# Performance work log

Hardware: AMD Instinct MI355X
Metric: run time of the kernel (lower is better)

Reference implementation:

```python
import jax, jax.numpy as jnp
import numpy as np

B, T, D, H, DH, W = 2, 2048, 512, 8, 64, 64  # batch, seq, d_model, heads, d_head, window
BASE = 10000.0


def rope(x):
    # x: [b, t, d]; rotate-half RoPE applied over the full feature dim (as in source: pos_enc on d_model)
    d = x.shape[-1]
    half = d // 2
    inv_freq = BASE ** (-jnp.arange(half, dtype=jnp.float32) / half)          # [half]
    ang = jnp.arange(x.shape[1], dtype=jnp.float32)[:, None] * inv_freq       # [t, half]
    cos, sin = jnp.cos(ang), jnp.sin(ang)
    x1, x2 = x[..., :half], x[..., half:]
    return jnp.concatenate([x1 * cos - x2 * sin, x1 * sin + x2 * cos], axis=-1)


def setup_inputs() -> dict:
    key = jax.random.key(0)
    k0, k1, k2, k3 = jax.random.split(key, 4)
    x = jax.random.normal(k0, (B, T, D), jnp.float32)
    Wq = jax.random.normal(k1, (D, D), jnp.float32) / jnp.sqrt(D)
    Wkv = jax.random.normal(k2, (D, 2 * D), jnp.float32) / jnp.sqrt(D)
    # NOTE: source zero-inits lin; we use random weights so the output/grads are non-trivial
    Wlin = jax.random.normal(k3, (D, D), jnp.float32) / jnp.sqrt(D)
    blin = jnp.zeros((D,), jnp.float32)
    return {"x": x, "Wq": Wq, "Wkv": Wkv, "Wlin": Wlin, "blin": blin}


def reference(x, Wq, Wkv, Wlin, blin):
    b, t, _ = x.shape
    scale = DH ** -0.5
    q = rope(x @ Wq).reshape(b, t, H, DH).transpose(0, 2, 1, 3)               # [b,h,t,d]
    kv = x @ Wkv
    k, v = kv[..., :D], kv[..., D:]
    k = rope(k).reshape(b, t, H, DH).transpose(0, 2, 1, 3)                    # [b,h,t,d]
    v = v.reshape(b, t, H, DH).transpose(0, 2, 1, 3)                          # [b,h,t,d]
    pad = [(0, 0), (0, 0), (W - 1, 0), (0, 0)]
    kp, vp = jnp.pad(k, pad), jnp.pad(v, pad)                                 # [b,h,t+W-1,d]
    idx = jnp.arange(t)[:, None] + jnp.arange(W)[None, :]                     # [t,W] sliding-window gather
    kw, vw = kp[:, :, idx], vp[:, :, idx]                                     # [b,h,t,W,d]
    attn = jax.nn.softmax(jnp.einsum('bhtd,bhtwd->bhtw', q, kw) * scale, axis=-1)
    out = jnp.einsum('bhtw,bhtwd->bhtd', attn, vw)                            # [b,h,t,d]
    out = out.transpose(0, 2, 1, 3).reshape(b, t, D)
    return out @ Wlin + blin
```

## Files before the change

kernel.cpp:

```cpp
#include <hip/hip_runtime.h>
#include <cstddef>

#define T_N 2048
#define D_N 512
#define H_N 8
#define M_N 4096
#define KP  512

typedef __attribute__((ext_vector_type(4))) float f32x4;
typedef _Float16 f16x8 __attribute__((ext_vector_type(8)));
typedef _Float16 f16x4 __attribute__((ext_vector_type(4)));

#define GLOAD_LDS(g, l) __builtin_amdgcn_global_load_lds( \
    (const __attribute__((address_space(1))) unsigned int*)(g), \
    (__attribute__((address_space(3))) unsigned int*)(l), 16, 0, 0)

__global__ __launch_bounds__(256) void trig_kernel(float* __restrict__ tab) {
  int idx = blockIdx.x * blockDim.x + threadIdx.x;
  int t = idx >> 8, f = idx & 255;
  float invf = exp2f(-0.05190512648261503f * (float)f);
  float ang = (float)t * invf;
  float s, c;
  sincosf(ang, &s, &c);
  tab[t * 512 + f] = c;
  tab[t * 512 + 256 + f] = s;
}

__global__ __launch_bounds__(256) void pack_all(
    const float* __restrict__ x, const float* __restrict__ Wq,
    const float* __restrict__ Wkv, const float* __restrict__ Wlin,
    _Float16* __restrict__ Axp, _Float16* __restrict__ Wcatp,
    _Float16* __restrict__ Wlinp) {
  __shared__ float tile[64][65];
  int bid = blockIdx.x;
  const int tid = threadIdx.x;
  if (bid < 1024) {
    int idx = bid * 256 + tid;
    int m = idx >> 6, k8 = (idx & 63) << 3;
    const float* src = x + (size_t)m * 512 + k8;
    const float4 a = *(const float4*)src;
    const float4 b = *(const float4*)(src + 4);
    f16x8 o;
    o[0] = (_Float16)a.x; o[1] = (_Float16)a.y; o[2] = (_Float16)a.z; o[3] = (_Float16)a.w;
    o[4] = (_Float16)b.x; o[5] = (_Float16)b.y; o[6] = (_Float16)b.z; o[7] = (_Float16)b.w;
    *(f16x8*)(Axp + (size_t)m * 512 + k8) = o;
    return;
  }
  bid -= 1024;
  const float* W; int N; _Float16* out; int bx, by;
  if (bid < 64)       { W = Wq;   N = 512;  out = Wcatp;                        bx = bid & 7;  by = bid >> 3; }
  else if (bid < 192) { bid -= 64;  W = Wkv; N = 1024; out = Wcatp + (size_t)512 * KP; bx = bid & 15; by = bid >> 4; }
  else                { bid -= 192; W = Wlin; N = 512; out = Wlinp;             bx = bid & 7;  by = bid >> 3; }
  const int n0 = bx * 64, k0 = by * 64;
#pragma unroll
  for (int it = 0; it < 16; ++it) {
    int idx = tid + it * 256;
    int r = idx >> 6, c = idx & 63;
    tile[r][c] = W[(size_t)(k0 + r) * N + n0 + c];
  }
  __syncthreads();
#pragma unroll
  for (int it = 0; it < 16; ++it) {
    int idx = tid + it * 256;
    int n = idx >> 6, kk = idx & 63;
    out[(size_t)(n0 + n) * KP + k0 + kk] = (_Float16)tile[kk][n];
  }
}

__global__ __launch_bounds__(256) void gemm_mfma(
    const _Float16* __restrict__ Ap, const _Float16* __restrict__ Bp,
    float* __restrict__ C, int ldc, const float* __restrict__ bias) {
  __shared__ __align__(16) _Float16 sA[128 * 64];
  __shared__ __align__(16) _Float16 sB[128 * 64];
  const int tid = threadIdx.x;
  const int wid = tid >> 6, lane = tid & 63;
  const int m0 = blockIdx.y * 128, n0 = blockIdx.x * 128;
  const int wm = (wid >> 1) * 64, wn = (wid & 1) * 64;
  f32x4 acc[4][4] = {};

  const int srow = wid * 32 + (lane >> 3);
  const int scol = (lane & 7) * 8;
  const _Float16* ga = Ap + (size_t)(m0 + srow) * KP + scol;
  const _Float16* gb = Bp + (size_t)(n0 + srow) * KP + scol;
  _Float16* la = &sA[wid * 32 * 64];
  _Float16* lb = &sB[wid * 32 * 64];

  for (int k0 = 0; k0 < KP; k0 += 64) {
#pragma unroll
    for (int i = 0; i < 4; ++i) {
      GLOAD_LDS(ga + (size_t)(i * 8) * KP + k0, la + i * 8 * 64);
      GLOAD_LDS(gb + (size_t)(i * 8) * KP + k0, lb + i * 8 * 64);
    }
    __syncthreads();
#pragma unroll
    for (int ks = 0; ks < 2; ++ks) {
      f16x8 af[4], bfr[4];
#pragma unroll
      for (int i = 0; i < 4; ++i) {
        af[i]  = *(const f16x8*)&sA[(wm + i * 16 + (lane & 15)) * 64 + ks * 32 + (lane >> 4) * 8];
        bfr[i] = *(const f16x8*)&sB[(wn + i * 16 + (lane & 15)) * 64 + ks * 32 + (lane >> 4) * 8];
      }
#pragma unroll
      for (int i = 0; i < 4; ++i)
#pragma unroll
        for (int j = 0; j < 4; ++j)
          acc[i][j] = __builtin_amdgcn_mfma_f32_16x16x32_f16(af[i], bfr[j], acc[i][j], 0, 0, 0);
    }
    __syncthreads();
  }
  const int cn = n0 + wn + (lane & 15);
  const int rbase = m0 + wm + (lane >> 4) * 4;
#pragma unroll
  for (int j = 0; j < 4; ++j) {
    float badd = bias ? bias[cn + j * 16] : 0.f;
#pragma unroll
    for (int i = 0; i < 4; ++i)
#pragma unroll
      for (int r = 0; r < 4; ++r)
        C[(size_t)(rbase + i * 16 + r) * ldc + cn + j * 16] = acc[i][j][r] + badd;
  }
}

__global__ __launch_bounds__(256) void rope_pack(
    const float* __restrict__ qkv, const float* __restrict__ tab,
    _Float16* __restrict__ Qh, _Float16* __restrict__ Kh,
    _Float16* __restrict__ Vh) {
  int bid = blockIdx.x;
  const int tid = threadIdx.x;
  if (bid < 2048) {
    int idx = bid * 256 + tid;
    int which = idx >> 18;
    int r = idx & ((1 << 18) - 1);
    int m = r >> 6;
    int c4 = (r & 63) << 2;
    int t = m & (T_N - 1);
    int b = m >> 11;
    const float* base = qkv + (size_t)m * 1536 + (which ? 512 : 0);
    const float4 v1 = *(const float4*)(base + c4);
    const float4 v2 = *(const float4*)(base + c4 + 256);
    const float4 ct = *(const float4*)(tab + (size_t)t * 512 + c4);
    const float4 st = *(const float4*)(tab + (size_t)t * 512 + 256 + c4);
    f16x4 o1, o2;
    o1[0] = (_Float16)(v1.x * ct.x - v2.x * st.x);  o2[0] = (_Float16)(v1.x * st.x + v2.x * ct.x);
    o1[1] = (_Float16)(v1.y * ct.y - v2.y * st.y);  o2[1] = (_Float16)(v1.y * st.y + v2.y * ct.y);
    o1[2] = (_Float16)(v1.z * ct.z - v2.z * st.z);  o2[2] = (_Float16)(v1.z * st.z + v2.z * ct.z);
    o1[3] = (_Float16)(v1.w * ct.w - v2.w * st.w);  o2[3] = (_Float16)(v1.w * st.w + v2.w * ct.w);
    _Float16* dst = which ? Kh : Qh;
    int h1 = c4 >> 6, d1 = c4 & 63;
    *(f16x4*)(dst + ((size_t)(b * 8 + h1) * T_N + t) * 64 + d1) = o1;
    *(f16x4*)(dst + ((size_t)(b * 8 + h1 + 4) * T_N + t) * 64 + d1) = o2;
    return;
  }
  bid -= 2048;
  __shared__ _Float16 vt[64][72];
  const int b = bid >> 8, h = (bid >> 5) & 7, tt = bid & 31;
  const int t0 = tt * 64;
#pragma unroll
  for (int it = 0; it < 16; ++it) {
    int idx = tid + it * 256;
    int tl = idx >> 6, d = idx & 63;
    vt[d][tl] = (_Float16)qkv[(size_t)(b * T_N + t0 + tl) * 1536 + 1024 + h * 64 + d];
  }
  __syncthreads();
#pragma unroll
  for (int it = 0; it < 2; ++it) {
    int idx = tid + it * 256;
    int d = idx >> 3, tc = (idx & 7) * 8;
    *(f16x8*)(Vh + ((size_t)(b * 8 + h) * 64 + d) * T_N + t0 + tc) =
        *(const f16x8*)&vt[d][tc];
  }
}

#define RQ 72
#define RK 72
#define RV 104
#define RP 104
#define RO 72

__global__ __launch_bounds__(256, 4) void attn_fused(
    const _Float16* __restrict__ Qh, const _Float16* __restrict__ Kh,
    const _Float16* __restrict__ Vh, _Float16* __restrict__ Aout) {
  __shared__ __align__(16) _Float16 sm[19200];
  __shared__ float pm[2][32];
  __shared__ float ps[2][32];
  _Float16* Ks  = sm;
  _Float16* Qs  = sm + 6912;
  _Float16* VTs = sm + 9216;
  _Float16* Ps  = sm + 15872;
  _Float16* OH  = sm;

  const int wgid = blockIdx.x;
  const int orig = (wgid & 7) * 128 + (wgid >> 3);
  const int tile = orig & 63;
  const int h = (orig >> 6) & 7;
  const int b = orig >> 9;
  const int t0 = tile * 32;
  const int tid = threadIdx.x;
  const size_t bh = (size_t)(b * 8 + h);

  {
    int i = tid >> 3, d8 = (tid & 7) * 8;
    *(f16x8*)(Qs + i * RQ + d8) =
        *(const f16x8*)(Qh + (bh * T_N + t0 + i) * 64 + d8);
  }
#pragma unroll
  for (int itn = 0; itn < 3; ++itn) {
    int c = tid + itn * 256;
    int jr = c >> 3, d8 = (c & 7) * 8;
    int p = t0 - 64 + jr;
    f16x8 o = {};
    if (p >= 0) o = *(const f16x8*)(Kh + (bh * T_N + p) * 64 + d8);
    *(f16x8*)(Ks + jr * RK + d8) = o;
  }
#pragma unroll
  for (int itn = 0; itn < 3; ++itn) {
    int c = tid + itn * 256;
    int d = c & 63, ci = c >> 6 + 0;
    ci = (c >> 6);
    int jr8 = ci * 8;
    int p8 = t0 - 64 + jr8;
    f16x8 o = {};
    if (p8 >= 0) o = *(const f16x8*)(Vh + (bh * 64 + d) * T_N + p8);
    *(f16x8*)(VTs + d * RV + jr8) = o;
  }
  __syncthreads();

  const int lane = tid & 63;
  const int il = lane & 15, g = lane >> 4;
  const int w = tid >> 6;
  const int it = w & 1, jh = w >> 1;
  const int i_q = 16 * it + il;

  f32x4 sacc[3] = {};
  {
    f16x8 qf0 = *(const f16x8*)(Qs + i_q * RQ + 8 * g);
    f16x8 qf1 = *(const f16x8*)(Qs + i_q * RQ + 32 + 8 * g);
#pragma unroll
    for (int jt = 0; jt < 3; ++jt) {
      int jrow = 16 * (3 * jh + jt) + il;
      f16x8 a0 = *(const f16x8*)(Ks + jrow * RK + 8 * g);
      f16x8 a1 = *(const f16x8*)(Ks + jrow * RK + 32 + 8 * g);
      sacc[jt] = __builtin_amdgcn_mfma_f32_16x16x32_f16(a0, qf0, sacc[jt], 0, 0, 0);
      sacc[jt] = __builtin_amdgcn_mfma_f32_16x16x32_f16(a1, qf1, sacc[jt], 0, 0, 0);
    }
  }
  float mx = -3e38f;
#pragma unroll
  for (int jt = 0; jt < 3; ++jt)
#pragma unroll
    for (int r = 0; r < 4; ++r) {
      int j = 16 * (3 * jh + jt) + 4 * g + r;
      int wv = j - 1 - i_q;
      if (wv >= 0 && wv < 64) mx = fmaxf(mx, sacc[jt][r]);
    }
  mx = fmaxf(mx, __shfl_xor(mx, 16));
  mx = fmaxf(mx, __shfl_xor(mx, 32));
  if (g == 0) pm[jh][i_q] = mx;
  __syncthreads();
  {
    const float m = fmaxf(pm[0][i_q], pm[1][i_q]);
    float sum = 0.f;
#pragma unroll
    for (int jt = 0; jt < 3; ++jt)
#pragma unroll
      for (int r = 0; r < 4; ++r) {
        int j = 16 * (3 * jh + jt) + 4 * g + r;
        int wv = j - 1 - i_q;
        float ex = 0.f;
        if (wv >= 0 && wv < 64) {
          ex = exp2f((sacc[jt][r] - m) * 0.18033688011112042f);
          sum += ex;
        }
        Ps[i_q * RP + j] = (_Float16)ex;
      }
    sum += __shfl_xor(sum, 16);
    sum += __shfl_xor(sum, 32);
    if (g == 0) ps[jh][i_q] = sum;
  }
  __syncthreads();

  f32x4 oacc[2] = {};
#pragma unroll
  for (int ks = 0; ks < 3; ++ks) {
    f16x8 pf = *(const f16x8*)(Ps + i_q * RP + 32 * ks + 8 * g);
#pragma unroll
    for (int q2 = 0; q2 < 2; ++q2) {
      int dt = jh + 2 * q2;
      f16x8 vf = *(const f16x8*)(VTs + (16 * dt + il) * RV + 32 * ks + 8 * g);
      oacc[q2] = __builtin_amdgcn_mfma_f32_16x16x32_f16(pf, vf, oacc[q2], 0, 0, 0);
    }
  }
#pragma unroll
  for (int r = 0; r < 4; ++r) {
    int i = 16 * it + 4 * g + r;
    float inv = 1.f / (ps[0][i] + ps[1][i]);
#pragma unroll
    for (int q2 = 0; q2 < 2; ++q2) {
      int d = 16 * (jh + 2 * q2) + il;
      OH[i * RO + d] = (_Float16)(oacc[q2][r] * inv);
    }
  }
  __syncthreads();
  {
    int i = tid >> 3, d8 = (tid & 7) * 8;
    *(f16x8*)(Aout + ((size_t)(b * T_N + t0 + i)) * 512 + h * 64 + d8) =
        *(const f16x8*)(OH + i * RO + d8);
  }
}

extern "C" void kernel_launch(void* const* d_in, const int* in_sizes, int n_in,
                              void* d_out, int out_size, void* d_ws, size_t ws_size,
                              hipStream_t stream) {
  const float* x    = (const float*)d_in[0];
  const float* Wq   = (const float*)d_in[1];
  const float* Wkv  = (const float*)d_in[2];
  const float* Wlin = (const float*)d_in[3];
  const float* blin = (const float*)d_in[4];
  float* out = (float*)d_out;

  char* ws = (char*)d_ws;
  float*     qkvbuf = (float*)(ws);
  float*     tab    = (float*)(ws + 25165824);
  _Float16*  Axp    = (_Float16*)(ws + 29360128);
  _Float16*  Wcatp  = (_Float16*)(ws + 33554432);
  _Float16*  Wlinp  = (_Float16*)(ws + 35127296);
  _Float16*  Qh     = (_Float16*)(ws + 35651584);
  _Float16*  Kh     = (_Float16*)(ws + 39845888);
  _Float16*  Vh     = (_Float16*)(ws + 44040192);
  _Float16*  Aaop   = (_Float16*)(ws + 48234496);

  trig_kernel<<<T_N, 256, 0, stream>>>(tab);
  pack_all<<<1280, 256, 0, stream>>>(x, Wq, Wkv, Wlin, Axp, Wcatp, Wlinp);
  gemm_mfma<<<dim3(12, 32), 256, 0, stream>>>(Axp, Wcatp, qkvbuf, 1536, nullptr);
  rope_pack<<<2560, 256, 0, stream>>>(qkvbuf, tab, Qh, Kh, Vh);
  attn_fused<<<1024, 256, 0, stream>>>(Qh, Kh, Vh, Aaop);
  gemm_mfma<<<dim3(4, 32), 256, 0, stream>>>(Aaop, Wlinp, out, 512, blin);
}
```

Baseline: 116.2 us.

## Fuse RoPE into QKV GEMM epilogue, merge trig into prep, shrink GEMM tiles

Permutes the Wq/Wk columns during weight packing so that each RoPE pair (f, f+256) sits in adjacent output columns. RoPE can then run in the QKV GEMM epilogue using a lane shuffle, writing fp16 Q/K head-major directly instead of going through an fp32 qkv buffer. The trig table is now fp16 and is generated inside the prep kernel, which removes one launch. V is written as fp16 and transposed by a separate small kernel. Both GEMMs use smaller tiles to put more blocks in flight. The risks are extra fp16 rounding in the sin/cos values and scattered 2-byte epilogue stores.

New measurement: 112.0 us. 1.04x faster.

```diff
diff --git a/kernel.cpp b/kernel.cpp
--- a/kernel.cpp
+++ b/kernel.cpp
@@ -2,37 +2,24 @@
 #include <cstddef>
 
 #define T_N 2048
-#define D_N 512
-#define H_N 8
 #define M_N 4096
-#define KP  512
+#define KW  512
 
 typedef __attribute__((ext_vector_type(4))) float f32x4;
 typedef _Float16 f16x8 __attribute__((ext_vector_type(8)));
-typedef _Float16 f16x4 __attribute__((ext_vector_type(4)));
+typedef _Float16 f16x2 __attribute__((ext_vector_type(2)));
 
 #define GLOAD_LDS(g, l) __builtin_amdgcn_global_load_lds( \
     (const __attribute__((address_space(1))) unsigned int*)(g), \
     (__attribute__((address_space(3))) unsigned int*)(l), 16, 0, 0)
 
-__global__ __launch_bounds__(256) void trig_kernel(float* __restrict__ tab) {
-  int idx = blockIdx.x * blockDim.x + threadIdx.x;
-  int t = idx >> 8, f = idx & 255;
-  float invf = exp2f(-0.05190512648261503f * (float)f);
-  float ang = (float)t * invf;
-  float s, c;
-  sincosf(ang, &s, &c);
-  tab[t * 512 + f] = c;
-  tab[t * 512 + 256 + f] = s;
-}
-
-__global__ __launch_bounds__(256) void pack_all(
+__global__ __launch_bounds__(256) void prep(
     const float* __restrict__ x, const float* __restrict__ Wq,
     const float* __restrict__ Wkv, const float* __restrict__ Wlin,
     _Float16* __restrict__ Axp, _Float16* __restrict__ Wcatp,
-    _Float16* __restrict__ Wlinp) {
+    _Float16* __restrict__ Wlinp, _Float16* __restrict__ tab16) {
   __shared__ float tile[64][65];
-  int bid = blockIdx.x;
+  const int bid = blockIdx.x;
   const int tid = threadIdx.x;
   if (bid < 1024) {
     int idx = bid * 256 + tid;
@@ -46,11 +33,22 @@
     *(f16x8*)(Axp + (size_t)m * 512 + k8) = o;
     return;
   }
-  bid -= 1024;
-  const float* W; int N; _Float16* out; int bx, by;
-  if (bid < 64)       { W = Wq;   N = 512;  out = Wcatp;                        bx = bid & 7;  by = bid >> 3; }
-  else if (bid < 192) { bid -= 64;  W = Wkv; N = 1024; out = Wcatp + (size_t)512 * KP; bx = bid & 15; by = bid >> 4; }
-  else                { bid -= 192; W = Wlin; N = 512; out = Wlinp;             bx = bid & 7;  by = bid >> 3; }
+  if (bid >= 1280) {
+    int gid = (bid - 1280) * 256 + tid;
+    int t = gid >> 8, f = gid & 255;
+    float invf = exp2f(-0.05190512648261503f * (float)f);
+    float s, c;
+    sincosf((float)t * invf, &s, &c);
+    f16x2 cs;
+    cs[0] = (_Float16)c; cs[1] = (_Float16)s;
+    *(f16x2*)(tab16 + 2 * ((size_t)t * 256 + f)) = cs;
+    return;
+  }
+  int wb = bid - 1024;
+  const float* W; int N; int mode; int bx, by;
+  if (wb < 64)       { W = Wq;   N = 512;  mode = 0; bx = wb & 7;  by = wb >> 3; }
+  else if (wb < 192) { wb -= 64;  W = Wkv; N = 1024; mode = 1; bx = wb & 15; by = wb >> 4; }
+  else               { wb -= 192; W = Wlin; N = 512; mode = 2; bx = wb & 7;  by = wb >> 3; }
   const int n0 = bx * 64, k0 = by * 64;
 #pragma unroll
   for (int it = 0; it < 16; ++it) {
@@ -63,103 +61,104 @@
   for (int it = 0; it < 16; ++it) {
     int idx = tid + it * 256;
     int n = idx >> 6, kk = idx & 63;
-    out[(size_t)(n0 + n) * KP + k0 + kk] = (_Float16)tile[kk][n];
-  }
-}
-
-__global__ __launch_bounds__(256) void gemm_mfma(
+    int cg = n0 + n;
+    int np; _Float16* out;
+    if (mode == 0)      { np = 2 * (cg & 255) + (cg >> 8); out = Wcatp; }
+    else if (mode == 1) { np = (cg < 512) ? 512 + 2 * (cg & 255) + (cg >> 8)
+                                          : 1024 + (cg - 512);
+                          out = Wcatp; }
+    else                { np = cg; out = Wlinp; }
+    out[(size_t)np * KW + k0 + kk] = (_Float16)tile[kk][n];
+  }
+}
+
+__global__ __launch_bounds__(256) void gemm_qkv_rope(
     const _Float16* __restrict__ Ap, const _Float16* __restrict__ Bp,
-    float* __restrict__ C, int ldc, const float* __restrict__ bias) {
-  __shared__ __align__(16) _Float16 sA[128 * 64];
+    const _Float16* __restrict__ tab16, _Float16* __restrict__ Qh,
+    _Float16* __restrict__ Kh, _Float16* __restrict__ Vn) {
+  __shared__ __align__(16) _Float16 sA[64 * 64];
   __shared__ __align__(16) _Float16 sB[128 * 64];
   const int tid = threadIdx.x;
   const int wid = tid >> 6, lane = tid & 63;
-  const int m0 = blockIdx.y * 128, n0 = blockIdx.x * 128;
-  const int wm = (wid >> 1) * 64, wn = (wid & 1) * 64;
-  f32x4 acc[4][4] = {};
-
-  const int srow = wid * 32 + (lane >> 3);
-  const int scol = (lane & 7) * 8;
-  const _Float16* ga = Ap + (size_t)(m0 + srow) * KP + scol;
-  const _Float16* gb = Bp + (size_t)(n0 + srow) * KP + scol;
-  _Float16* la = &sA[wid * 32 * 64];
-  _Float16* lb = &sB[wid * 32 * 64];
-
-  for (int k0 = 0; k0 < KP; k0 += 64) {
-#pragma unroll
-    for (int i = 0; i < 4; ++i) {
-      GLOAD_LDS(ga + (size_t)(i * 8) * KP + k0, la + i * 8 * 64);
-      GLOAD_LDS(gb + (size_t)(i * 8) * KP + k0, lb + i * 8 * 64);
-    }
+  const int il = lane & 15, g = lane >> 4;
+  const int m0 = blockIdx.y * 64, n0 = blockIdx.x * 128;
+  const int wm = (wid >> 1) * 32, wn = (wid & 1) * 64;
+  f32x4 acc[2][4] = {};
+
+  const _Float16* ga = Ap + (size_t)(m0 + wid * 16 + (lane >> 3)) * KW + (lane & 7) * 8;
+  const _Float16* gb = Bp + (size_t)(n0 + wid * 32 + (lane >> 3)) * KW + (lane & 7) * 8;
+  _Float16* la = sA + wid * 16 * 64;
+  _Float16* lb = sB + wid * 32 * 64;
+
+  for (int k0 = 0; k0 < KW; k0 += 64) {
+    GLOAD_LDS(ga + k0, la);
+    GLOAD_LDS(ga + 8 * KW + k0, la + 8 * 64);
+#pragma unroll
+    for (int p = 0; p < 4; ++p)
+      GLOAD_LDS(gb + (size_t)(p * 8) * KW + k0, lb + p * 8 * 64);
     __syncthreads();
 #pragma unroll
     for (int ks = 0; ks < 2; ++ks) {
-      f16x8 af[4], bfr[4];
-#pragma unroll
-      for (int i = 0; i < 4; ++i) {
-        af[i]  = *(const f16x8*)&sA[(wm + i * 16 + (lane & 15)) * 64 + ks * 32 + (lane >> 4) * 8];
-        bfr[i] = *(const f16x8*)&sB[(wn + i * 16 + (lane & 15)) * 64 + ks * 32 + (lane >> 4) * 8];
+      f16x8 af[2], bf[4];
+#pragma unroll
+      for (int i = 0; i < 2; ++i)
+        af[i] = *(const f16x8*)&sA[(wm + i * 16 + il) * 64 + ks * 32 + g * 8];
+#pragma unroll
+      for (int j = 0; j < 4; ++j)
+        bf[j] = *(const f16x8*)&sB[(wn + j * 16 + il) * 64 + ks * 32 + g * 8];
+#pragma unroll
+      for (int i = 0; i < 2; ++i)
+#pragma unroll
+        for (int j = 0; j < 4; ++j)
+          acc[i][j] = __builtin_amdgcn_mfma_f32_16x16x32_f16(af[i], bf[j], acc[i][j], 0, 0, 0);
+    }
+    __syncthreads();
+  }
+  const int b8 = (m0 >> 11) * 8;
+  const bool isv = (n0 >= 1024);
+  const bool isk = (n0 >= 512) && !isv;
+  const int n0p = n0 - (isk ? 512 : 0);
+#pragma unroll
+  for (int i = 0; i < 2; ++i) {
+#pragma unroll
+    for (int j = 0; j < 4; ++j) {
+      f32x4 v = acc[i][j];
+#pragma unroll
+      for (int r = 0; r < 4; ++r) {
+        float self = v[r];
+        float part = __shfl_xor(self, 1);
+        int tl = wm + i * 16 + g * 4 + r;
+        int tpos = (m0 + tl) & (T_N - 1);
+        if (isv) {
+          Vn[(size_t)(m0 + tl) * 512 + (n0 - 1024) + wn + il + 16 * j] = (_Float16)self;
+        } else {
+          int p = il & 1;
+          int f = (n0p + wn + 16 * j + (il & 14)) >> 1;
+          f16x2 cs = *(const f16x2*)(tab16 + 2 * ((size_t)tpos * 256 + f));
+          float c = (float)cs[0], s = (float)cs[1];
+          float o = p ? (self * c + part * s) : (self * c - part * s);
+          int h = (f >> 6) + (p << 2);
+          int d = f & 63;
+          _Float16* dst = isk ? Kh : Qh;
+          dst[((size_t)(b8 + h) * T_N + tpos) * 64 + d] = (_Float16)o;
+        }
       }
-#pragma unroll
-      for (int i = 0; i < 4; ++i)
-#pragma unroll
-        for (int j = 0; j < 4; ++j)
-          acc[i][j] = __builtin_amdgcn_mfma_f32_16x16x32_f16(af[i], bfr[j], acc[i][j], 0, 0, 0);
-    }
-    __syncthreads();
-  }
-  const int cn = n0 + wn + (lane & 15);
-  const int rbase = m0 + wm + (lane >> 4) * 4;
-#pragma unroll
-  for (int j = 0; j < 4; ++j) {
-    float badd = bias ? bias[cn + j * 16] : 0.f;
-#pragma unroll
-    for (int i = 0; i < 4; ++i)
-#pragma unroll
-      for (int r = 0; r < 4; ++r)
-        C[(size_t)(rbase + i * 16 + r) * ldc + cn + j * 16] = acc[i][j][r] + badd;
-  }
-}
-
-__global__ __launch_bounds__(256) void rope_pack(
-    const float* __restrict__ qkv, const float* __restrict__ tab,
-    _Float16* __restrict__ Qh, _Float16* __restrict__ Kh,
-    _Float16* __restrict__ Vh) {
-  int bid = blockIdx.x;
-  const int tid = threadIdx.x;
-  if (bid < 2048) {
-    int idx = bid * 256 + tid;
-    int which = idx >> 18;
-    int r = idx & ((1 << 18) - 1);
-    int m = r >> 6;
-    int c4 = (r & 63) << 2;
-    int t = m & (T_N - 1);
-    int b = m >> 11;
-    const float* base = qkv + (size_t)m * 1536 + (which ? 512 : 0);
-    const float4 v1 = *(const float4*)(base + c4);
-    const float4 v2 = *(const float4*)(base + c4 + 256);
-    const float4 ct = *(const float4*)(tab + (size_t)t * 512 + c4);
-    const float4 st = *(const float4*)(tab + (size_t)t * 512 + 256 + c4);
-    f16x4 o1, o2;
-    o1[0] = (_Float16)(v1.x * ct.x - v2.x * st.x);  o2[0] = (_Float16)(v1.x * st.x + v2.x * ct.x);
-    o1[1] = (_Float16)(v1.y * ct.y - v2.y * st.y);  o2[1] = (_Float16)(v1.y * st.y + v2.y * ct.y);
-    o1[2] = (_Float16)(v1.z * ct.z - v2.z * st.z);  o2[2] = (_Float16)(v1.z * st.z + v2.z * ct.z);
-    o1[3] = (_Float16)(v1.w * ct.w - v2.w * st.w);  o2[3] = (_Float16)(v1.w * st.w + v2.w * ct.w);
-    _Float16* dst = which ? Kh : Qh;
-    int h1 = c4 >> 6, d1 = c4 & 63;
-    *(f16x4*)(dst + ((size_t)(b * 8 + h1) * T_N + t) * 64 + d1) = o1;
-    *(f16x4*)(dst + ((size_t)(b * 8 + h1 + 4) * T_N + t) * 64 + d1) = o2;
-    return;
-  }
-  bid -= 2048;
+    }
+  }
+}
+
+__global__ __launch_bounds__(256) void vtrans(
+    const _Float16* __restrict__ Vn, _Float16* __restrict__ Vh) {
   __shared__ _Float16 vt[64][72];
+  const int bid = blockIdx.x;
+  const int tid = threadIdx.x;
   const int b = bid >> 8, h = (bid >> 5) & 7, tt = bid & 31;
   const int t0 = tt * 64;
 #pragma unroll
   for (int it = 0; it < 16; ++it) {
     int idx = tid + it * 256;
     int tl = idx >> 6, d = idx & 63;
-    vt[d][tl] = (_Float16)qkv[(size_t)(b * T_N + t0 + tl) * 1536 + 1024 + h * 64 + d];
+    vt[d][tl] = Vn[(size_t)(b * T_N + t0 + tl) * 512 + h * 64 + d];
   }
   __syncthreads();
 #pragma unroll
@@ -215,9 +214,7 @@
 #pragma unroll
   for (int itn = 0; itn < 3; ++itn) {
     int c = tid + itn * 256;
-    int d = c & 63, ci = c >> 6 + 0;
-    ci = (c >> 6);
-    int jr8 = ci * 8;
+    int d = c & 63, jr8 = (c >> 6) * 8;
     int p8 = t0 - 64 + jr8;
     f16x8 o = {};
     if (p8 >= 0) o = *(const f16x8*)(Vh + (bh * 64 + d) * T_N + p8);
@@ -308,6 +305,59 @@
   }
 }
 
+__global__ __launch_bounds__(256) void gemm_out(
+    const _Float16* __restrict__ Ap, const _Float16* __restrict__ Bp,
+    const float* __restrict__ bias, float* __restrict__ C) {
+  __shared__ __align__(16) _Float16 sA[64 * 64];
+  __shared__ __align__(16) _Float16 sB[64 * 64];
+  const int tid = threadIdx.x;
+  const int wid = tid >> 6, lane = tid & 63;
+  const int il = lane & 15, g = lane >> 4;
+  const int m0 = blockIdx.y * 64, n0 = blockIdx.x * 64;
+  const int wm = (wid >> 1) * 32, wn = (wid & 1) * 32;
+  f32x4 acc[2][2] = {};
+
+  const _Float16* ga = Ap + (size_t)(m0 + wid * 16 + (lane >> 3)) * KW + (lane & 7) * 8;
+  const _Float16* gb = Bp + (size_t)(n0 + wid * 16 + (lane >> 3)) * KW + (lane & 7) * 8;
+  _Float16* la = sA + wid * 16 * 64;
+  _Float16* lb = sB + wid * 16 * 64;
+
+  for (int k0 = 0; k0 < KW; k0 += 64) {
+    GLOAD_LDS(ga + k0, la);
+    GLOAD_LDS(ga + 8 * KW + k0, la + 8 * 64);
+    GLOAD_LDS(gb + k0, lb);
+    GLOAD_LDS(gb + 8 * KW + k0, lb + 8 * 64);
+    __syncthreads();
+#pragma unroll
+    for (int ks = 0; ks < 2; ++ks) {
+      f16x8 af[2], bf[2];
+#pragma unroll
+      for (int i = 0; i < 2; ++i)
+        af[i] = *(const f16x8*)&sA[(wm + i * 16 + il) * 64 + ks * 32 + g * 8];
+#pragma unroll
+      for (int j = 0; j < 2; ++j)
+        bf[j] = *(const f16x8*)&sB[(wn + j * 16 + il) * 64 + ks * 32 + g * 8];
+#pragma unroll
+      for (int i = 0; i < 2; ++i)
+#pragma unroll
+        for (int j = 0; j < 2; ++j)
+          acc[i][j] = __builtin_amdgcn_mfma_f32_16x16x32_f16(af[i], bf[j], acc[i][j], 0, 0, 0);
+    }
+    __syncthreads();
+  }
+  const int cn = n0 + wn + il;
+  const int rbase = m0 + wm + g * 4;
+#pragma unroll
+  for (int j = 0; j < 2; ++j) {
+    float badd = bias[cn + j * 16];
+#pragma unroll
+    for (int i = 0; i < 2; ++i)
+#pragma unroll
+      for (int r = 0; r < 4; ++r)
+        C[(size_t)(rbase + i * 16 + r) * 512 + cn + j * 16] = acc[i][j][r] + badd;
+  }
+}
+
 extern "C" void kernel_launch(void* const* d_in, const int* in_sizes, int n_in,
                               void* d_out, int out_size, void* d_ws, size_t ws_size,
                               hipStream_t stream) {
@@ -319,20 +369,19 @@
   float* out = (float*)d_out;
 
   char* ws = (char*)d_ws;
-  float*     qkvbuf = (float*)(ws);
-  float*     tab    = (float*)(ws + 25165824);
-  _Float16*  Axp    = (_Float16*)(ws + 29360128);
-  _Float16*  Wcatp  = (_Float16*)(ws + 33554432);
-  _Float16*  Wlinp  = (_Float16*)(ws + 35127296);
-  _Float16*  Qh     = (_Float16*)(ws + 35651584);
-  _Float16*  Kh     = (_Float16*)(ws + 39845888);
-  _Float16*  Vh     = (_Float16*)(ws + 44040192);
-  _Float16*  Aaop   = (_Float16*)(ws + 48234496);
-
-  trig_kernel<<<T_N, 256, 0, stream>>>(tab);
-  pack_all<<<1280, 256, 0, stream>>>(x, Wq, Wkv, Wlin, Axp, Wcatp, Wlinp);
-  gemm_mfma<<<dim3(12, 32), 256, 0, stream>>>(Axp, Wcatp, qkvbuf, 1536, nullptr);
-  rope_pack<<<2560, 256, 0, stream>>>(qkvbuf, tab, Qh, Kh, Vh);
+  _Float16* Axp   = (_Float16*)(ws);
+  _Float16* Wcatp = (_Float16*)(ws + 4194304);
+  _Float16* Wlinp = (_Float16*)(ws + 5767168);
+  _Float16* tab16 = (_Float16*)(ws + 6291456);
+  _Float16* Qh    = (_Float16*)(ws + 8388608);
+  _Float16* Kh    = (_Float16*)(ws + 12582912);
+  _Float16* Vn    = (_Float16*)(ws + 16777216);
+  _Float16* Vh    = (_Float16*)(ws + 20971520);
+  _Float16* Aaop  = (_Float16*)(ws + 25165824);
+
+  prep<<<3328, 256, 0, stream>>>(x, Wq, Wkv, Wlin, Axp, Wcatp, Wlinp, tab16);
+  gemm_qkv_rope<<<dim3(12, 64), 256, 0, stream>>>(Axp, Wcatp, tab16, Qh, Kh, Vn);
+  vtrans<<<512, 256, 0, stream>>>(Vn, Vh);
   attn_fused<<<1024, 256, 0, stream>>>(Qh, Kh, Vh, Aaop);
-  gemm_mfma<<<dim3(4, 32), 256, 0, stream>>>(Aaop, Wlinp, out, 512, blin);
-}
+  gemm_out<<<dim3(8, 64), 256, 0, stream>>>(Aaop, Wlinp, blin, out);
+}
```
